# Performance work log

Measured on AMD Instinct MI355X. Metric: run time of the kernel, lower is better.

## Reference

```python
import jax, jax.numpy as jnp
import numpy as np

B, N_INP, N_HID = 524288, 32, 256
NE, NI = 200, 56                      # excitatory / inhibitory columns, NE+NI == N_HID
W_E, W_I = 0.5, 0.5
WIN_E, WIN_I = 1.0, 1.0
RHO = 0.9                             # target spectral radius of h2h
DT, RC, BIAS = 0.01, 1.0, 0.0
THRESHOLD, RESET = 1.0, 0.0
LEAKY_BETA, LEAKY_THRESH = 0.9, 1.0   # snn.Leaky(beta=0.9) defaults


def setup_inputs() -> dict:
    key = jax.random.key(0)
    kx, kx2h, ke, ki = jax.random.split(key, 4)
    x = jax.random.normal(kx, (B, N_INP), dtype=jnp.float32)

    # x2h: uniform(0,1) scaled columnwise by [win_e]*Ne ++ [win_i]*Ni
    col_scale = jnp.concatenate([jnp.full((NE,), WIN_E), jnp.full((NI,), WIN_I)]).astype(jnp.float32)
    x2h = jax.random.uniform(kx2h, (N_INP, N_HID), dtype=jnp.float32) * col_scale

    # h2h: [w_e*U(0,1) | -w_i*U(0,1)] then rescaled to spectral radius RHO
    h2h_e = W_E * jax.random.uniform(ke, (N_HID, NE), dtype=jnp.float32)
    h2h_i = -W_I * jax.random.uniform(ki, (N_HID, NI), dtype=jnp.float32)
    h2h = jnp.concatenate([h2h_e, h2h_i], axis=1)
    eig_max = np.max(np.abs(np.linalg.eigvals(np.asarray(h2h, dtype=np.float64))))
    h2h = (h2h * (RHO / eig_max)).astype(jnp.float32)

    return {"x": x, "x2h": x2h, "h2h": h2h}


def reference(x, x2h, h2h):
    # forward() unsqueezes a length-1 time axis, so the LIF loop runs exactly once
    # with zero-initialized states. NOTE arg swap in the original call:
    # LIFcell(x, hy, u) called as LIFcell(x_t, u_state, hy_state):
    #   - spike/threshold/reset acts on hy_state (zeros)
    #   - recurrent matmul uses u_state (zeros)
    u_state = jnp.zeros((x.shape[0], h2h.shape[0]), dtype=x.dtype)   # [B, n_hid]
    hy_state = jnp.zeros_like(u_state)

    spk = (hy_state > THRESHOLD).astype(x.dtype)
    hy_state = jnp.where(spk == 1.0, RESET, hy_state)

    u_dot = -hy_state + (u_state @ h2h + x @ x2h + BIAS)             # [B, n_hid]
    u = hy_state + u_dot * (RC * DT)

    # hy = snn.Leaky(u)[0] is computed in the original but appended to hy_list,
    # which is never returned, so it does not affect the outputs.
    return (u, spk)
```

## Files before the change

### kernel.cpp

```cpp
#include <hip/hip_runtime.h>
#include <stdint.h>


#define NHID 256
#define NINP 32
#define RPC  8

typedef float __attribute__((ext_vector_type(4))) f32x4;

__device__ __forceinline__ void stage_chunk(const float* src_lane, void* lds_wave_base) {
    __builtin_amdgcn_global_load_lds(
        (const __attribute__((address_space(1))) uint32_t*)src_lane,
        (__attribute__((address_space(3))) uint32_t*)lds_wave_base,
        16, 0, 0);
}

__global__ __launch_bounds__(256) void lsm_u_kernel(
    const float* __restrict__ x, const float* __restrict__ x2h,
    float* __restrict__ u, int B, int nwaves)
{
    __shared__ float xbuf[4][2][RPC * NINP];

    const int lane = threadIdx.x & 63;
    const int wv   = threadIdx.x >> 6;
    const int wid  = __builtin_amdgcn_readfirstlane(blockIdx.x * 4 + wv);

    const int c = lane * 4;
    f32x4 w[NINP];
#pragma unroll
    for (int k = 0; k < NINP; ++k) {
        f32x4 t = *reinterpret_cast<const f32x4*>(x2h + k * NHID + c);
        w[k] = t * 0.01f;
    }

    const int total_chunks = B / RPC;
    const int nch = (total_chunks - wid + nwaves - 1) / nwaves;
    if (nch <= 0) return;

    const float* src0 = x + (size_t)wid * (RPC * NINP) + lane * 4;
    const size_t src_stride = (size_t)nwaves * (RPC * NINP);

    stage_chunk(src0, &xbuf[wv][0][0]);
    if (nch > 1) stage_chunk(src0 + src_stride, &xbuf[wv][1][0]);

    for (int i = 0; i < nch; ++i) {
        if (i == 0) {
            if (nch > 1) asm volatile("s_waitcnt vmcnt(1)" ::: "memory");
            else         asm volatile("s_waitcnt vmcnt(0)" ::: "memory");
        } else if (i == nch - 1) {
            asm volatile("s_waitcnt vmcnt(8)" ::: "memory");
        } else {
            asm volatile("s_waitcnt vmcnt(9)" ::: "memory");
        }

        const float* xb = &xbuf[wv][i & 1][0];
        const size_t row0 = ((size_t)wid + (size_t)i * nwaves) * RPC;

#pragma unroll 2
        for (int r = 0; r < RPC; ++r) {
            const f32x4* xr = (const f32x4*)(xb + r * NINP);
            f32x4 acc = {0.f, 0.f, 0.f, 0.f};
#pragma unroll
            for (int g = 0; g < 8; ++g) {
                f32x4 xq = xr[g];
                acc += w[4 * g + 0] * xq.x;
                acc += w[4 * g + 1] * xq.y;
                acc += w[4 * g + 2] * xq.z;
                acc += w[4 * g + 3] * xq.w;
            }
            __builtin_nontemporal_store(acc, (f32x4*)(u + (row0 + r) * NHID + c));
        }

        if (i + 2 < nch) stage_chunk(src0 + (size_t)(i + 2) * src_stride, &xbuf[wv][i & 1][0]);
    }
}

extern "C" void kernel_launch(void* const* d_in, const int* in_sizes, int n_in,
                              void* d_out, int out_size, void* d_ws, size_t ws_size,
                              hipStream_t stream) {
    const float* x   = (const float*)d_in[0];
    const float* x2h = (const float*)d_in[1];

    const int B = in_sizes[0] / NINP;
    float* u   = (float*)d_out;
    float* spk = u + (size_t)B * NHID;

    hipMemsetAsync(spk, 0, (size_t)B * NHID * sizeof(float), stream);

    const int threads = 256;
    const int blocks  = 2048;
    const int nwaves  = blocks * (threads / 64);
    lsm_u_kernel<<<blocks, threads, 0, stream>>>(x, x2h, u, B, nwaves);
}
```

Baseline: 225.1 us.

## Add dedicated producer wave, fuse spk zero-fill, switch to per-column scalar layout

```diff
diff --git a/kernel.cpp b/kernel.cpp
--- a/kernel.cpp
+++ b/kernel.cpp
@@ -5,61 +5,57 @@
 #define NHID 256
 #define NINP 32
 #define RPC  8
+#define NBUF 4
+#define BLOCKS 2048
 
 typedef float __attribute__((ext_vector_type(4))) f32x4;
 
-__device__ __forceinline__ void stage_chunk(const float* src_lane, void* lds_wave_base) {
+__device__ __forceinline__ void stage_chunk(const float* src_lane, void* lds_base) {
     __builtin_amdgcn_global_load_lds(
         (const __attribute__((address_space(1))) uint32_t*)src_lane,
-        (__attribute__((address_space(3))) uint32_t*)lds_wave_base,
+        (__attribute__((address_space(3))) uint32_t*)lds_base,
         16, 0, 0);
 }
 
-__global__ __launch_bounds__(256) void lsm_u_kernel(
+__global__ __launch_bounds__(320) void lsm_kernel(
     const float* __restrict__ x, const float* __restrict__ x2h,
-    float* __restrict__ u, int B, int nwaves)
+    float* __restrict__ u, float* __restrict__ spk, int B)
 {
-    __shared__ float xbuf[4][2][RPC * NINP];
+    __shared__ float xbuf[NBUF][RPC * NINP];
 
     const int lane = threadIdx.x & 63;
     const int wv   = threadIdx.x >> 6;
-    const int wid  = __builtin_amdgcn_readfirstlane(blockIdx.x * 4 + wv);
+    const int nch  = (B / RPC) / BLOCKS;
+    const size_t chunk0 = (size_t)blockIdx.x * nch;
 
-    const int c = lane * 4;
-    f32x4 w[NINP];
-#pragma unroll
-    for (int k = 0; k < NINP; ++k) {
-        f32x4 t = *reinterpret_cast<const f32x4*>(x2h + k * NHID + c);
-        w[k] = t * 0.01f;
+    if (wv == 4) {
+        const float* src = x + chunk0 * (RPC * NINP) + lane * 4;
+        const size_t stride = RPC * NINP;
+        stage_chunk(src, &xbuf[0][0]);
+        if (nch > 1) stage_chunk(src + stride, &xbuf[1][0]);
+        for (int k = 0; k < nch; ++k) {
+            if (k + 2 < nch) stage_chunk(src + (size_t)(k + 2) * stride, &xbuf[(k + 2) & 3][0]);
+            if (k + 2 < nch)      asm volatile("s_waitcnt vmcnt(2)" ::: "memory");
+            else if (k + 1 < nch) asm volatile("s_waitcnt vmcnt(1)" ::: "memory");
+            else                  asm volatile("s_waitcnt vmcnt(0)" ::: "memory");
+            asm volatile("s_barrier" ::: "memory");
+        }
+        return;
     }
 
-    const int total_chunks = B / RPC;
-    const int nch = (total_chunks - wid + nwaves - 1) / nwaves;
-    if (nch <= 0) return;
+    const int c = wv * 64 + lane;
+    float w[NINP];
+#pragma unroll
+    for (int k = 0; k < NINP; ++k) w[k] = x2h[k * NHID + c] * 0.01f;
 
-    const float* src0 = x + (size_t)wid * (RPC * NINP) + lane * 4;
-    const size_t src_stride = (size_t)nwaves * (RPC * NINP);
-
-    stage_chunk(src0, &xbuf[wv][0][0]);
-    if (nch > 1) stage_chunk(src0 + src_stride, &xbuf[wv][1][0]);
-
-    for (int i = 0; i < nch; ++i) {
-        if (i == 0) {
-            if (nch > 1) asm volatile("s_waitcnt vmcnt(1)" ::: "memory");
-            else         asm volatile("s_waitcnt vmcnt(0)" ::: "memory");
-        } else if (i == nch - 1) {
-            asm volatile("s_waitcnt vmcnt(8)" ::: "memory");
-        } else {
-            asm volatile("s_waitcnt vmcnt(9)" ::: "memory");
-        }
-
-        const float* xb = &xbuf[wv][i & 1][0];
-        const size_t row0 = ((size_t)wid + (size_t)i * nwaves) * RPC;
-
-#pragma unroll 2
+    for (int k = 0; k < nch; ++k) {
+        asm volatile("s_barrier" ::: "memory");
+        const float* xb = &xbuf[k & 3][0];
+        const size_t row0 = (chunk0 + k) * RPC;
+#pragma unroll
         for (int r = 0; r < RPC; ++r) {
             const f32x4* xr = (const f32x4*)(xb + r * NINP);
-            f32x4 acc = {0.f, 0.f, 0.f, 0.f};
+            float acc = 0.f;
 #pragma unroll
             for (int g = 0; g < 8; ++g) {
                 f32x4 xq = xr[g];
@@ -68,10 +64,10 @@
                 acc += w[4 * g + 2] * xq.z;
                 acc += w[4 * g + 3] * xq.w;
             }
-            __builtin_nontemporal_store(acc, (f32x4*)(u + (row0 + r) * NHID + c));
+            const size_t base = (row0 + r) * NHID + c;
+            __builtin_nontemporal_store(acc, u + base);
+            __builtin_nontemporal_store(0.f, spk + base);
         }
-
-        if (i + 2 < nch) stage_chunk(src0 + (size_t)(i + 2) * src_stride, &xbuf[wv][i & 1][0]);
     }
 }
 
@@ -85,10 +81,5 @@
     float* u   = (float*)d_out;
     float* spk = u + (size_t)B * NHID;
 
-    hipMemsetAsync(spk, 0, (size_t)B * NHID * sizeof(float), stream);
-
-    const int threads = 256;
-    const int blocks  = 2048;
-    const int nwaves  = blocks * (threads / 64);
-    lsm_u_kernel<<<blocks, threads, 0, stream>>>(x, x2h, u, B, nwaves);
+    lsm_kernel<<<BLOCKS, 320, 0, stream>>>(x, x2h, u, spk, B);
 }
```

Measured after the change: 226.6 us. Within noise of the previous version (+0.7%).
